# Kernel optimization log

Hardware: AMD Instinct MI355X
Metric: run time of the kernel (lower is better)

## Reference

```python
import jax, jax.numpy as jnp
import numpy as np

N = 8192
IN_F = 512
OUT_F = 64
ALPHA = 0.2  # LeakyReLU negative slope
NEG_INF = -9e15


def setup_inputs() -> dict:
    key = jax.random.key(0)
    k1, k2, k3, k4 = jax.random.split(key, 4)
    x = jax.random.normal(k1, (N, IN_F), dtype=jnp.float32)
    adj = jax.random.randint(k2, (N, N), 0, 2, dtype=jnp.int32)
    # xavier_uniform with gain=1.414
    def xavier(k, shape, gain=1.414):
        fan_in, fan_out = shape[0], shape[1]
        a = gain * np.sqrt(6.0 / (fan_in + fan_out))
        return jax.random.uniform(k, shape, jnp.float32, -a, a)
    W = xavier(k3, (IN_F, OUT_F))
    a = xavier(k4, (2 * OUT_F, 1))
    return {"x": x, "adj": adj, "W": W, "a": a}


def reference(x, adj, W, a):
    h = x @ W  # [N, F]
    f = W.shape[1]
    # e[i,j] = leakyrelu([h_i, h_j] @ a) = leakyrelu(h_i@a1 + h_j@a2)
    e1 = h @ a[:f, 0]   # [N]
    e2 = h @ a[f:, 0]   # [N]
    e = jax.nn.leaky_relu(e1[:, None] + e2[None, :], negative_slope=ALPHA)  # [N, N]
    scores = jnp.where(adj > 0, e, NEG_INF)
    attention = jax.nn.softmax(scores, axis=1)  # dropout p=0.0 -> identity
    h_prime = attention @ h  # [N, F]
    return jax.nn.elu(h_prime)  # concat=True
```

## Files before the change

### kernel.cpp

```cpp
#include <hip/hip_runtime.h>
#include <hip/hip_bf16.h>

#define NN 8192
#define KF 512
#define FF 64
#define GAT_ALPHA 0.2f
#define MSHIFT 20.0f
#define LOG2E 1.44269504f

#define JSPLIT 4
#define JCH 512
#define NCHB (NN / JSPLIT / JCH)
#define PST 520

#define EXP2F(x) __builtin_amdgcn_exp2f(x)

typedef __attribute__((ext_vector_type(8))) __bf16 bf16x8;
typedef __attribute__((ext_vector_type(4))) float f32x4;

__global__ __launch_bounds__(256) void zero_ws(float4* __restrict__ p) {
    p[blockIdx.x * 256 + threadIdx.x] = make_float4(0.f, 0.f, 0.f, 0.f);
}

__global__ __launch_bounds__(256) void gat_linear(
    const float* __restrict__ x, const float* __restrict__ W,
    const float* __restrict__ av, __hip_bfloat16* __restrict__ ht,
    float* __restrict__ e1, float* __restrict__ e2)
{
    __shared__ float xs[32][33];
    __shared__ float Ws[32][64];
    __shared__ float ep[2][32][17];

    const int t  = threadIdx.x;
    const int fq = t & 15;
    const int rq = t >> 4;
    const int i0 = blockIdx.x * 32;

    const int kl = t & 31, r0 = t >> 5;
    const int fw = t & 63, kq = t >> 6;

    float acc[2][4] = {};

    for (int kt = 0; kt < KF; kt += 32) {
        #pragma unroll
        for (int m = 0; m < 4; ++m)
            xs[kl][r0 + 8 * m] = x[(size_t)(i0 + r0 + 8 * m) * KF + kt + kl];
        #pragma unroll
        for (int m = 0; m < 8; ++m)
            Ws[kq + 4 * m][fw] = W[(size_t)(kt + kq + 4 * m) * FF + fw];
        __syncthreads();
        #pragma unroll
        for (int kk = 0; kk < 32; ++kk) {
            float x0 = xs[kk][rq * 2];
            float x1 = xs[kk][rq * 2 + 1];
            f32x4 wv = *(const f32x4*)&Ws[kk][fq * 4];
            #pragma unroll
            for (int v = 0; v < 4; ++v) {
                acc[0][v] += x0 * wv[v];
                acc[1][v] += x1 * wv[v];
            }
        }
        __syncthreads();
    }

    #pragma unroll
    for (int v = 0; v < 4; ++v) {
        int f = fq * 4 + v;
        union { ushort2 q; __hip_bfloat16 h[2]; } pk;
        pk.h[0] = __float2bfloat16(acc[0][v]);
        pk.h[1] = __float2bfloat16(acc[1][v]);
        *(ushort2*)&ht[(size_t)f * NN + i0 + rq * 2] = pk.q;
    }

    f32x4 a1v = *(const f32x4*)&av[fq * 4];
    f32x4 a2v = *(const f32x4*)&av[64 + fq * 4];
    #pragma unroll
    for (int u = 0; u < 2; ++u) {
        float s1 = 0.f, s2 = 0.f;
        #pragma unroll
        for (int v = 0; v < 4; ++v) {
            s1 += acc[u][v] * a1v[v];
            s2 += acc[u][v] * a2v[v];
        }
        ep[0][rq * 2 + u][fq] = s1;
        ep[1][rq * 2 + u][fq] = s2;
    }
    __syncthreads();
    if (t < 32) {
        float s1 = 0.f, s2 = 0.f;
        #pragma unroll
        for (int q = 0; q < 16; ++q) { s1 += ep[0][t][q]; s2 += ep[1][t][q]; }
        e1[i0 + t] = s1 * LOG2E;
        e2[i0 + t] = s2 * LOG2E;
    }
}

__global__ __launch_bounds__(256, 8) void gat_attn(
    const int* __restrict__ adj, const __hip_bfloat16* __restrict__ ht,
    const float* __restrict__ e1, const float* __restrict__ e2,
    float* __restrict__ acc, float* __restrict__ lsum)
{
    __shared__ __hip_bfloat16 ps[16][PST];
    __shared__ float l_red[16];

    const int t     = threadIdx.x;
    const int ii    = t >> 4;
    const int jq    = t & 15;
    const int i0    = (blockIdx.x >> 2) * 16;
    const int jbase = (blockIdx.x & 3) * (NN / JSPLIT);
    const int lane  = t & 63;
    const int wv    = t >> 6;
    const int n16   = lane & 15;
    const int quad  = lane >> 4;

    const float e1L = e1[i0 + ii];
    float ms = e1L + MSHIFT * LOG2E;
    const float miL = ms > 0.f ? ms : GAT_ALPHA * ms;

    if (t < 16) l_red[t] = 0.f;

    const int*   arow = adj + (size_t)(i0 + ii) * NN + jbase + jq * 4;
    const float* e2p  = e2 + jbase + jq * 4;
    const __hip_bfloat16* hbase = ht + (size_t)(wv * 16 + n16) * NN + jbase + quad * 8;

    int4 aj[8];
    #pragma unroll
    for (int g = 0; g < 8; ++g)
        aj[g] = *(const int4*)(arow + g * 64);

    float lpart = 0.f;
    f32x4 dacc = {0.f, 0.f, 0.f, 0.f};

    for (int c = 0; c < NCHB; ++c) {
        #pragma unroll
        for (int g = 0; g < 8; ++g) {
            float4 e_ = *(const float4*)(e2p + c * JCH + g * 64);
            int4   a_ = aj[g];
            union { uint2 u; __hip_bfloat16 h[4]; } pk;
            float s_, p_;
            s_ = e1L + e_.x; s_ = s_ > 0.f ? s_ : GAT_ALPHA * s_;
            p_ = a_.x > 0 ? EXP2F(s_ - miL) : 0.f;
            pk.h[0] = __float2bfloat16(p_); lpart += __bfloat162float(pk.h[0]);
            s_ = e1L + e_.y; s_ = s_ > 0.f ? s_ : GAT_ALPHA * s_;
            p_ = a_.y > 0 ? EXP2F(s_ - miL) : 0.f;
            pk.h[1] = __float2bfloat16(p_); lpart += __bfloat162float(pk.h[1]);
            s_ = e1L + e_.z; s_ = s_ > 0.f ? s_ : GAT_ALPHA * s_;
            p_ = a_.z > 0 ? EXP2F(s_ - miL) : 0.f;
            pk.h[2] = __float2bfloat16(p_); lpart += __bfloat162float(pk.h[2]);
            s_ = e1L + e_.w; s_ = s_ > 0.f ? s_ : GAT_ALPHA * s_;
            p_ = a_.w > 0 ? EXP2F(s_ - miL) : 0.f;
            pk.h[3] = __float2bfloat16(p_); lpart += __bfloat162float(pk.h[3]);
            *(uint2*)&ps[ii][g * 64 + jq * 4] = pk.u;
        }
        if (c + 1 < NCHB) {
            #pragma unroll
            for (int g = 0; g < 8; ++g)
                aj[g] = *(const int4*)(arow + (c + 1) * JCH + g * 64);
        }
        __syncthreads();
        const __hip_bfloat16* hb = hbase + (size_t)c * JCH;
        #pragma unroll
        for (int kk = 0; kk < JCH / 32; ++kk) {
            bf16x8 af = *(const bf16x8*)&ps[n16][kk * 32 + quad * 8];
            bf16x8 bf = *(const bf16x8*)(hb + kk * 32);
            dacc = __builtin_amdgcn_mfma_f32_16x16x32_bf16(af, bf, dacc, 0, 0, 0);
        }
        __syncthreads();
    }

    atomicAdd(&l_red[ii], lpart);
    __syncthreads();
    if (t < 16) atomicAdd(&lsum[i0 + t], l_red[t]);

    #pragma unroll
    for (int r = 0; r < 4; ++r) {
        int row = quad * 4 + r;
        atomicAdd(&acc[(size_t)(i0 + row) * FF + wv * 16 + n16], dacc[r]);
    }
}

__global__ __launch_bounds__(256) void gat_epilogue(
    const float* __restrict__ acc, const float* __restrict__ lsum,
    float* __restrict__ out)
{
    int idx = (blockIdx.x * 256 + threadIdx.x) * 4;
    float li = 1.f / lsum[idx >> 6];
    f32x4 a = *(const f32x4*)(acc + idx);
    f32x4 o;
    #pragma unroll
    for (int v = 0; v < 4; ++v) {
        float hv = a[v] * li;
        o[v] = hv > 0.f ? hv : __expf(hv) - 1.f;
    }
    *(f32x4*)(out + idx) = o;
}

extern "C" void kernel_launch(void* const* d_in, const int* in_sizes, int n_in,
                              void* d_out, int out_size, void* d_ws, size_t ws_size,
                              hipStream_t stream) {
    const float* x   = (const float*)d_in[0];
    const int*   adj = (const int*)d_in[1];
    const float* W   = (const float*)d_in[2];
    const float* av  = (const float*)d_in[3];
    float* out = (float*)d_out;

    char* wsb = (char*)d_ws;
    __hip_bfloat16* ht = (__hip_bfloat16*)wsb;
    float* e1  = (float*)(wsb + (1 << 20));
    float* e2  = e1 + NN;
    float* acc = e2 + NN;
    float* lsum = acc + (size_t)NN * FF;

    zero_ws<<<(NN * FF + NN) / 1024, 256, 0, stream>>>((float4*)acc);
    gat_linear<<<256, 256, 0, stream>>>(x, W, av, ht, e1, e2);
    gat_attn<<<NN / 16 * JSPLIT, 256, 0, stream>>>(adj, ht, e1, e2, acc, lsum);
    gat_epilogue<<<NN * FF / 1024, 256, 0, stream>>>(acc, lsum, out);
}
```

Before: 430.0 us.

## Compute attention probabilities in MFMA register layout, drop LDS and atomics

Restructures the attention kernel so each wave builds its bf16 probability A-fragment directly in registers, matching the MFMA operand layout. This removes the shared-memory staging and the block barriers. Each wave now covers 16 rows by all 64 features with four accumulators, and adj, e2 and h loads are double-buffered one step ahead. The j-dimension split rises to 16, with partial sums written to separate per-split buffers that the epilogue reduces, replacing the atomics and the zeroing kernel. The cost is more workspace, extra epilogue reads, and more register pressure, which forces lower occupancy.

```diff
diff --git a/kernel.cpp b/kernel.cpp
--- a/kernel.cpp
+++ b/kernel.cpp
@@ -8,19 +8,14 @@
 #define MSHIFT 20.0f
 #define LOG2E 1.44269504f
 
-#define JSPLIT 4
-#define JCH 512
-#define NCHB (NN / JSPLIT / JCH)
-#define PST 520
+#define JSPLIT 16
+#define JW (NN / JSPLIT)
+#define KSTEPS (JW / 32)
 
 #define EXP2F(x) __builtin_amdgcn_exp2f(x)
 
 typedef __attribute__((ext_vector_type(8))) __bf16 bf16x8;
 typedef __attribute__((ext_vector_type(4))) float f32x4;
-
-__global__ __launch_bounds__(256) void zero_ws(float4* __restrict__ p) {
-    p[blockIdx.x * 256 + threadIdx.x] = make_float4(0.f, 0.f, 0.f, 0.f);
-}
 
 __global__ __launch_bounds__(256) void gat_linear(
     const float* __restrict__ x, const float* __restrict__ W,
@@ -95,97 +90,104 @@
     }
 }
 
-__global__ __launch_bounds__(256, 8) void gat_attn(
+__global__ __launch_bounds__(256, 4) void gat_attn(
     const int* __restrict__ adj, const __hip_bfloat16* __restrict__ ht,
     const float* __restrict__ e1, const float* __restrict__ e2,
-    float* __restrict__ acc, float* __restrict__ lsum)
+    float* __restrict__ accs, float* __restrict__ lsums)
 {
-    __shared__ __hip_bfloat16 ps[16][PST];
-    __shared__ float l_red[16];
-
     const int t     = threadIdx.x;
-    const int ii    = t >> 4;
-    const int jq    = t & 15;
-    const int i0    = (blockIdx.x >> 2) * 16;
-    const int jbase = (blockIdx.x & 3) * (NN / JSPLIT);
     const int lane  = t & 63;
     const int wv    = t >> 6;
     const int n16   = lane & 15;
     const int quad  = lane >> 4;
-
-    const float e1L = e1[i0 + ii];
+    const int split = blockIdx.x & (JSPLIT - 1);
+    const int i0    = (blockIdx.x >> 4) * 64 + wv * 16;
+    const int j0    = split * JW;
+    const int row   = i0 + n16;
+
+    const float e1L = e1[row];
     float ms = e1L + MSHIFT * LOG2E;
     const float miL = ms > 0.f ? ms : GAT_ALPHA * ms;
 
-    if (t < 16) l_red[t] = 0.f;
-
-    const int*   arow = adj + (size_t)(i0 + ii) * NN + jbase + jq * 4;
-    const float* e2p  = e2 + jbase + jq * 4;
-    const __hip_bfloat16* hbase = ht + (size_t)(wv * 16 + n16) * NN + jbase + quad * 8;
-
-    int4 aj[8];
-    #pragma unroll
-    for (int g = 0; g < 8; ++g)
-        aj[g] = *(const int4*)(arow + g * 64);
-
+    const int*            ap  = adj + (size_t)row * NN + j0 + quad * 8;
+    const float*          epx = e2 + j0 + quad * 8;
+    const __hip_bfloat16* hp  = ht + (size_t)n16 * NN + j0 + quad * 8;
+
+    int4   aA[2][2];
+    float4 eA[2][2];
+    bf16x8 bA[2][4];
     float lpart = 0.f;
-    f32x4 dacc = {0.f, 0.f, 0.f, 0.f};
-
-    for (int c = 0; c < NCHB; ++c) {
-        #pragma unroll
-        for (int g = 0; g < 8; ++g) {
-            float4 e_ = *(const float4*)(e2p + c * JCH + g * 64);
-            int4   a_ = aj[g];
-            union { uint2 u; __hip_bfloat16 h[4]; } pk;
-            float s_, p_;
-            s_ = e1L + e_.x; s_ = s_ > 0.f ? s_ : GAT_ALPHA * s_;
-            p_ = a_.x > 0 ? EXP2F(s_ - miL) : 0.f;
-            pk.h[0] = __float2bfloat16(p_); lpart += __bfloat162float(pk.h[0]);
-            s_ = e1L + e_.y; s_ = s_ > 0.f ? s_ : GAT_ALPHA * s_;
-            p_ = a_.y > 0 ? EXP2F(s_ - miL) : 0.f;
-            pk.h[1] = __float2bfloat16(p_); lpart += __bfloat162float(pk.h[1]);
-            s_ = e1L + e_.z; s_ = s_ > 0.f ? s_ : GAT_ALPHA * s_;
-            p_ = a_.z > 0 ? EXP2F(s_ - miL) : 0.f;
-            pk.h[2] = __float2bfloat16(p_); lpart += __bfloat162float(pk.h[2]);
-            s_ = e1L + e_.w; s_ = s_ > 0.f ? s_ : GAT_ALPHA * s_;
-            p_ = a_.w > 0 ? EXP2F(s_ - miL) : 0.f;
-            pk.h[3] = __float2bfloat16(p_); lpart += __bfloat162float(pk.h[3]);
-            *(uint2*)&ps[ii][g * 64 + jq * 4] = pk.u;
+    f32x4 dacc[4] = {{0.f,0.f,0.f,0.f},{0.f,0.f,0.f,0.f},{0.f,0.f,0.f,0.f},{0.f,0.f,0.f,0.f}};
+
+#define LOADB(sl, st)                                                         \
+    {                                                                         \
+        aA[sl][0] = *(const int4*)(ap + (st) * 32);                           \
+        aA[sl][1] = *(const int4*)(ap + (st) * 32 + 4);                       \
+        eA[sl][0] = *(const float4*)(epx + (st) * 32);                        \
+        eA[sl][1] = *(const float4*)(epx + (st) * 32 + 4);                    \
+        bA[sl][0] = *(const bf16x8*)(hp + (size_t)(st) * 32);                 \
+        bA[sl][1] = *(const bf16x8*)(hp + (size_t)16 * NN + (st) * 32);       \
+        bA[sl][2] = *(const bf16x8*)(hp + (size_t)32 * NN + (st) * 32);       \
+        bA[sl][3] = *(const bf16x8*)(hp + (size_t)48 * NN + (st) * 32);       \
+    }
+
+    LOADB(0, 0)
+    LOADB(1, 1)
+
+    #pragma unroll
+    for (int st = 0; st < KSTEPS; ++st) {
+        const int sl = st & 1;
+        union { bf16x8 v; __hip_bfloat16 h[8]; } af;
+        const int*   av4 = (const int*)&aA[sl][0];
+        const float* ev4 = (const float*)&eA[sl][0];
+        #pragma unroll
+        for (int jj = 0; jj < 8; ++jj) {
+            float s_ = e1L + ev4[jj];
+            s_ = s_ > 0.f ? s_ : GAT_ALPHA * s_;
+            float p_ = av4[jj] > 0 ? EXP2F(s_ - miL) : 0.f;
+            af.h[jj] = __float2bfloat16(p_);
+            lpart += __bfloat162float(af.h[jj]);
         }
-        if (c + 1 < NCHB) {
-            #pragma unroll
-            for (int g = 0; g < 8; ++g)
-                aj[g] = *(const int4*)(arow + (c + 1) * JCH + g * 64);
-        }
-        __syncthreads();
-        const __hip_bfloat16* hb = hbase + (size_t)c * JCH;
-        #pragma unroll
-        for (int kk = 0; kk < JCH / 32; ++kk) {
-            bf16x8 af = *(const bf16x8*)&ps[n16][kk * 32 + quad * 8];
-            bf16x8 bf = *(const bf16x8*)(hb + kk * 32);
-            dacc = __builtin_amdgcn_mfma_f32_16x16x32_bf16(af, bf, dacc, 0, 0, 0);
-        }
-        __syncthreads();
-    }
-
-    atomicAdd(&l_red[ii], lpart);
-    __syncthreads();
-    if (t < 16) atomicAdd(&lsum[i0 + t], l_red[t]);
-
-    #pragma unroll
-    for (int r = 0; r < 4; ++r) {
-        int row = quad * 4 + r;
-        atomicAdd(&acc[(size_t)(i0 + row) * FF + wv * 16 + n16], dacc[r]);
-    }
+        bf16x8 b0 = bA[sl][0], b1 = bA[sl][1], b2 = bA[sl][2], b3 = bA[sl][3];
+        if (st + 2 < KSTEPS) LOADB(sl, st + 2)
+        dacc[0] = __builtin_amdgcn_mfma_f32_16x16x32_bf16(af.v, b0, dacc[0], 0, 0, 0);
+        dacc[1] = __builtin_amdgcn_mfma_f32_16x16x32_bf16(af.v, b1, dacc[1], 0, 0, 0);
+        dacc[2] = __builtin_amdgcn_mfma_f32_16x16x32_bf16(af.v, b2, dacc[2], 0, 0, 0);
+        dacc[3] = __builtin_amdgcn_mfma_f32_16x16x32_bf16(af.v, b3, dacc[3], 0, 0, 0);
+    }
+#undef LOADB
+
+    lpart += __shfl_xor(lpart, 16);
+    lpart += __shfl_xor(lpart, 32);
+    if (quad == 0) lsums[(size_t)split * NN + row] = lpart;
+
+    float* ab = accs + (size_t)split * NN * FF;
+    #pragma unroll
+    for (int ft = 0; ft < 4; ++ft)
+        #pragma unroll
+        for (int r = 0; r < 4; ++r)
+            ab[(size_t)(i0 + quad * 4 + r) * FF + ft * 16 + n16] = dacc[ft][r];
 }
 
 __global__ __launch_bounds__(256) void gat_epilogue(
-    const float* __restrict__ acc, const float* __restrict__ lsum,
+    const float* __restrict__ accs, const float* __restrict__ lsums,
     float* __restrict__ out)
 {
-    int idx = (blockIdx.x * 256 + threadIdx.x) * 4;
-    float li = 1.f / lsum[idx >> 6];
-    f32x4 a = *(const f32x4*)(acc + idx);
+    const int idx = (blockIdx.x * 256 + threadIdx.x) * 4;
+    const int row = idx >> 6;
+
+    float l = 0.f;
+    #pragma unroll
+    for (int s = 0; s < JSPLIT; ++s) l += lsums[(size_t)s * NN + row];
+
+    f32x4 a = {0.f, 0.f, 0.f, 0.f};
+    #pragma unroll
+    for (int s = 0; s < JSPLIT; ++s) {
+        f32x4 v = *(const f32x4*)(accs + (size_t)s * NN * FF + idx);
+        a.x += v.x; a.y += v.y; a.z += v.z; a.w += v.w;
+    }
+
+    const float li = 1.f / l;
     f32x4 o;
     #pragma unroll
     for (int v = 0; v < 4; ++v) {
@@ -206,13 +208,12 @@
 
     char* wsb = (char*)d_ws;
     __hip_bfloat16* ht = (__hip_bfloat16*)wsb;
-    float* e1  = (float*)(wsb + (1 << 20));
-    float* e2  = e1 + NN;
-    float* acc = e2 + NN;
-    float* lsum = acc + (size_t)NN * FF;
-
-    zero_ws<<<(NN * FF + NN) / 1024, 256, 0, stream>>>((float4*)acc);
+    float* e1    = (float*)(wsb + (1 << 20));
+    float* e2    = e1 + NN;
+    float* accs  = e2 + NN;
+    float* lsums = accs + (size_t)JSPLIT * NN * FF;
+
     gat_linear<<<256, 256, 0, stream>>>(x, W, av, ht, e1, e2);
-    gat_attn<<<NN / 16 * JSPLIT, 256, 0, stream>>>(adj, ht, e1, e2, acc, lsum);
-    gat_epilogue<<<NN * FF / 1024, 256, 0, stream>>>(acc, lsum, out);
-}
+    gat_attn<<<(NN / 64) * JSPLIT, 256, 0, stream>>>(adj, ht, e1, e2, accs, lsums);
+    gat_epilogue<<<NN * FF / 1024, 256, 0, stream>>>(accs, lsums, out);
+}
```

Result: no change. 427.5 us (-0.6%).
